# Kernel optimization log

Hardware: AMD Instinct MI355X
Metric: run time of the kernel (lower is better)

Reference implementation:

```python
import jax, jax.numpy as jnp
import numpy as np

D_MODEL = 512
NUM_HEADS = 8
HEAD_DIM = D_MODEL // NUM_HEADS
NUM_Z_BINS = 16
MAX_Z = 5.0
N = 2048


def setup_inputs() -> dict:
    key = jax.random.key(0)
    ks = jax.random.split(key, 12)
    s = 1.0 / np.sqrt(D_MODEL)
    return {
        "x": jax.random.normal(ks[0], (N, D_MODEL), dtype=jnp.float32),
        "z_matrix": jax.random.uniform(ks[1], (N, N), dtype=jnp.float32),
        "Wq": jax.random.normal(ks[2], (D_MODEL, D_MODEL), dtype=jnp.float32) * s,
        "bq": jnp.zeros((D_MODEL,), dtype=jnp.float32),
        "Wk": jax.random.normal(ks[3], (D_MODEL, D_MODEL), dtype=jnp.float32) * s,
        "bk": jnp.zeros((D_MODEL,), dtype=jnp.float32),
        "Wv": jax.random.normal(ks[4], (D_MODEL, D_MODEL), dtype=jnp.float32) * s,
        "bv": jnp.zeros((D_MODEL,), dtype=jnp.float32),
        "Wo": jax.random.normal(ks[5], (D_MODEL, D_MODEL), dtype=jnp.float32) * s,
        "bo": jnp.zeros((D_MODEL,), dtype=jnp.float32),
        "z_table": jax.random.normal(ks[6], (NUM_Z_BINS, NUM_HEADS), dtype=jnp.float32) * 0.02,
    }


def reference(x, z_matrix, Wq, bq, Wk, bk, Wv, bv, Wo, bo, z_table):
    n = x.shape[0]
    scale = HEAD_DIM ** -0.5
    q = (x @ Wq + bq).reshape(n, NUM_HEADS, HEAD_DIM)
    k = (x @ Wk + bk).reshape(n, NUM_HEADS, HEAD_DIM)
    v = (x @ Wv + bv).reshape(n, NUM_HEADS, HEAD_DIM)
    # [n, h, m] attention scores
    scores = jnp.einsum('nhd,mhd->nhm', q, k) * scale
    # Z-bus relative bias: bin pairwise z values into NUM_Z_BINS over [0, MAX_Z],
    # look up per-head bias from the embedding table.
    bins = jnp.clip(jnp.floor(z_matrix / MAX_Z * NUM_Z_BINS).astype(jnp.int32), 0, NUM_Z_BINS - 1)
    bias = z_table[bins]                    # [n, n, h]
    scores = scores + jnp.transpose(bias, (0, 2, 1))  # [n, h, n]
    attn = jax.nn.softmax(scores, axis=-1)  # dropout p=0.0 (eval)
    out = jnp.einsum('nhm,mhd->nhd', attn, v).reshape(n, D_MODEL)
    return out @ Wo + bo
```

## Files before the change

### kernel.cpp

```cpp
#include <hip/hip_runtime.h>
#include <hip/hip_bf16.h>


#define NTOK   2048
#define DM     512
#define NH     8
#define DH     64
#define NBINS  16
#define NSPLIT 4
#define KPS    (NTOK / NSPLIT)

typedef float  f32x16 __attribute__((ext_vector_type(16)));
typedef short  short8 __attribute__((ext_vector_type(8)));
typedef unsigned short ushort_t;

#define MFMA32(A, B, C) __builtin_amdgcn_mfma_f32_32x32x16_bf16((A), (B), (C), 0, 0, 0)

__device__ __forceinline__ ushort_t f2bf(float x) {
    __hip_bfloat16 h = __float2bfloat16(x);
    union { __hip_bfloat16 b; ushort_t u; } v; v.b = h;
    return v.u;
}
__device__ __forceinline__ float bf2f(ushort_t b) {
    union { unsigned u; float f; } v; v.u = ((unsigned)b) << 16;
    return v.f;
}
__device__ __forceinline__ void splitbf(float x, ushort_t& hi, ushort_t& lo) {
    hi = f2bf(x);
    lo = f2bf(x - bf2f(hi));
}

union FragU { unsigned u[4]; short8 s; };

__device__ __forceinline__ int z_to_bin(float z) {
    int b = (int)floorf(z / 5.0f * 16.0f);
    return b < 0 ? 0 : (b > 15 ? 15 : b);
}

__global__ __launch_bounds__(256)
void prep_all(const float* __restrict__ z, unsigned char* __restrict__ bins,
              const float* __restrict__ x, ushort_t* __restrict__ xh, ushort_t* __restrict__ xl,
              const float* __restrict__ Wq, const float* __restrict__ Wk,
              const float* __restrict__ Wv, const float* __restrict__ Wo,
              ushort_t* __restrict__ wt_hi_base, ushort_t* __restrict__ wt_lo_base) {
    const int bid = blockIdx.x;
    const int t   = threadIdx.x;
    __shared__ float Tl[32][33];

    if (bid < 4096) {
        int i = (bid * 256 + t) * 4;
        float4 zv = *reinterpret_cast<const float4*>(z + i);
        uchar4 b;
        b.x = (unsigned char)z_to_bin(zv.x);
        b.y = (unsigned char)z_to_bin(zv.y);
        b.z = (unsigned char)z_to_bin(zv.z);
        b.w = (unsigned char)z_to_bin(zv.w);
        *reinterpret_cast<uchar4*>(bins + i) = b;
    } else if (bid < 5120) {
        int i = ((bid - 4096) * 256 + t) * 4;
        float4 v = *reinterpret_cast<const float4*>(x + i);
        ushort_t h[4], l[4];
        splitbf(v.x, h[0], l[0]); splitbf(v.y, h[1], l[1]);
        splitbf(v.z, h[2], l[2]); splitbf(v.w, h[3], l[3]);
        *reinterpret_cast<ushort4*>(xh + i) = make_ushort4(h[0], h[1], h[2], h[3]);
        *reinterpret_cast<ushort4*>(xl + i) = make_ushort4(l[0], l[1], l[2], l[3]);
    } else {
        const int pz  = bid - 5120;
        const int zz  = pz >> 8;
        const int rem = pz & 255;
        const float* __restrict__ W = zz == 0 ? Wq : zz == 1 ? Wk : zz == 2 ? Wv : Wo;
        ushort_t* __restrict__ th = wt_hi_base + (size_t)zz * DM * DM * 2;
        ushort_t* __restrict__ tl = wt_lo_base + (size_t)zz * DM * DM * 2;
        const int r0 = (rem >> 4) * 32;
        const int c0 = (rem & 15) * 32;
        {
            const int r = t >> 3, c4 = (t & 7) * 4;
            float4 v = *reinterpret_cast<const float4*>(W + (size_t)(r0 + r) * DM + c0 + c4);
            Tl[r][c4 + 0] = v.x; Tl[r][c4 + 1] = v.y; Tl[r][c4 + 2] = v.z; Tl[r][c4 + 3] = v.w;
        }
        __syncthreads();
        {
            const int c = t >> 3, r4 = (t & 7) * 4;
            ushort_t h4[4], l4[4];
            #pragma unroll
            for (int k = 0; k < 4; ++k) splitbf(Tl[r4 + k][c], h4[k], l4[k]);
            *reinterpret_cast<ushort4*>(th + (size_t)(c0 + c) * DM + r0 + r4) =
                make_ushort4(h4[0], h4[1], h4[2], h4[3]);
            *reinterpret_cast<ushort4*>(tl + (size_t)(c0 + c) * DM + r0 + r4) =
                make_ushort4(l4[0], l4[1], l4[2], l4[3]);
        }
    }
}

__global__ __launch_bounds__(256, 3)
void qkv_gemm_mfma(const ushort_t* __restrict__ x_hi, const ushort_t* __restrict__ x_lo,
                   const ushort_t* __restrict__ wqt_hi, const ushort_t* __restrict__ wqt_lo,
                   const ushort_t* __restrict__ wkt_hi, const ushort_t* __restrict__ wkt_lo,
                   const ushort_t* __restrict__ wvt_hi, const ushort_t* __restrict__ wvt_lo,
                   const float* __restrict__ bq, const float* __restrict__ bk,
                   const float* __restrict__ bv,
                   ushort_t* __restrict__ q_hi, ushort_t* __restrict__ q_lo,
                   ushort_t* __restrict__ k_hi, ushort_t* __restrict__ k_lo,
                   ushort_t* __restrict__ vT_hi, ushort_t* __restrict__ vT_lo) {
    const int z = blockIdx.z;
    const ushort_t* __restrict__ bt_hi = z == 0 ? wqt_hi : z == 1 ? wkt_hi : wvt_hi;
    const ushort_t* __restrict__ bt_lo = z == 0 ? wqt_lo : z == 1 ? wkt_lo : wvt_lo;
    const float*    __restrict__ bias  = z == 0 ? bq : z == 1 ? bk : bv;

    const int n0 = blockIdx.x * 64;
    const int m0 = blockIdx.y * 64;
    const int t  = threadIdx.x;
    const int wid = t >> 6, l = t & 63, hf = l >> 5, lq = l & 31;
    const int wm = wid >> 1, wn = wid & 1;

    __shared__ __align__(16) ushort_t Ash_hi[64 * 40], Ash_lo[64 * 40];
    __shared__ __align__(16) ushort_t Bsh_hi[64 * 40], Bsh_lo[64 * 40];

    f32x16 acc;
    #pragma unroll
    for (int i = 0; i < 16; ++i) acc[i] = 0.0f;

    const int sr = t >> 2, sc = t & 3;

    uint4 ra_h, ra_l, rb_h, rb_l;
    auto LOAD = [&](int k0) {
        ra_h = *reinterpret_cast<const uint4*>(&x_hi[(size_t)(m0 + sr) * DM + k0 + 8 * sc]);
        ra_l = *reinterpret_cast<const uint4*>(&x_lo[(size_t)(m0 + sr) * DM + k0 + 8 * sc]);
        rb_h = *reinterpret_cast<const uint4*>(&bt_hi[(size_t)(n0 + sr) * DM + k0 + 8 * sc]);
        rb_l = *reinterpret_cast<const uint4*>(&bt_lo[(size_t)(n0 + sr) * DM + k0 + 8 * sc]);
    };
    LOAD(0);

    for (int k0 = 0; k0 < DM; k0 += 32) {
        __syncthreads();
        *reinterpret_cast<uint4*>(&Ash_hi[sr * 40 + 8 * sc]) = ra_h;
        *reinterpret_cast<uint4*>(&Ash_lo[sr * 40 + 8 * sc]) = ra_l;
        *reinterpret_cast<uint4*>(&Bsh_hi[sr * 40 + 8 * sc]) = rb_h;
        *reinterpret_cast<uint4*>(&Bsh_lo[sr * 40 + 8 * sc]) = rb_l;
        __syncthreads();
        if (k0 + 32 < DM) LOAD(k0 + 32);

        __builtin_amdgcn_s_setprio(1);
        #pragma unroll
        for (int kp = 0; kp < 2; ++kp) {
            const int co = 8 * (hf + 2 * kp);
            short8 ah = *reinterpret_cast<const short8*>(&Ash_hi[(32 * wm + lq) * 40 + co]);
            short8 al = *reinterpret_cast<const short8*>(&Ash_lo[(32 * wm + lq) * 40 + co]);
            short8 bh = *reinterpret_cast<const short8*>(&Bsh_hi[(32 * wn + lq) * 40 + co]);
            short8 bl = *reinterpret_cast<const short8*>(&Bsh_lo[(32 * wn + lq) * 40 + co]);
            acc = MFMA32(ah, bh, acc);
            acc = MFMA32(ah, bl, acc);
            acc = MFMA32(al, bh, acc);
        }
        __builtin_amdgcn_s_setprio(0);
    }

    const int nl = lq + 32 * wn;
    const float bval = bias[n0 + nl];
    const int hh = n0 >> 6;

    #pragma unroll
    for (int r = 0; r < 16; ++r) {
        const int ml = (r & 3) + 8 * (r >> 2) + 4 * hf + 32 * wm;
        const float v = acc[r] + bval;
        ushort_t hi, lo; splitbf(v, hi, lo);
        if (z < 2) {
            ushort_t* dh = z == 0 ? q_hi : k_hi;
            ushort_t* dl = z == 0 ? q_lo : k_lo;
            const size_t o = ((size_t)hh * NTOK + m0 + ml) * DH + nl;
            dh[o] = hi; dl[o] = lo;
        } else {
            const size_t o = ((size_t)hh * DH + nl) * NTOK + m0 + ml;
            vT_hi[o] = hi; vT_lo[o] = lo;
        }
    }
}

__global__ __launch_bounds__(256, 3)
void wo_gemm_mfma(const ushort_t* __restrict__ a_hi, const ushort_t* __restrict__ a_lo,
                  const ushort_t* __restrict__ bt_hi, const ushort_t* __restrict__ bt_lo,
                  const float* __restrict__ bias, float* __restrict__ out) {
    const int n0 = blockIdx.x * 64;
    const int m0 = blockIdx.y * 64;
    const int t  = threadIdx.x;
    const int wid = t >> 6, l = t & 63, hf = l >> 5, lq = l & 31;
    const int wm = wid >> 1, wn = wid & 1;

    __shared__ __align__(16) ushort_t Ash_hi[64 * 40], Ash_lo[64 * 40];
    __shared__ __align__(16) ushort_t Bsh_hi[64 * 40], Bsh_lo[64 * 40];

    f32x16 acc;
    #pragma unroll
    for (int i = 0; i < 16; ++i) acc[i] = 0.0f;

    const int sr = t >> 2, sc = t & 3;

    uint4 ra_h, ra_l, rb_h, rb_l;
    auto LOAD = [&](int k0) {
        ra_h = *reinterpret_cast<const uint4*>(&a_hi[(size_t)(m0 + sr) * DM + k0 + 8 * sc]);
        ra_l = *reinterpret_cast<const uint4*>(&a_lo[(size_t)(m0 + sr) * DM + k0 + 8 * sc]);
        rb_h = *reinterpret_cast<const uint4*>(&bt_hi[(size_t)(n0 + sr) * DM + k0 + 8 * sc]);
        rb_l = *reinterpret_cast<const uint4*>(&bt_lo[(size_t)(n0 + sr) * DM + k0 + 8 * sc]);
    };
    LOAD(0);

    for (int k0 = 0; k0 < DM; k0 += 32) {
        __syncthreads();
        *reinterpret_cast<uint4*>(&Ash_hi[sr * 40 + 8 * sc]) = ra_h;
        *reinterpret_cast<uint4*>(&Ash_lo[sr * 40 + 8 * sc]) = ra_l;
        *reinterpret_cast<uint4*>(&Bsh_hi[sr * 40 + 8 * sc]) = rb_h;
        *reinterpret_cast<uint4*>(&Bsh_lo[sr * 40 + 8 * sc]) = rb_l;
        __syncthreads();
        if (k0 + 32 < DM) LOAD(k0 + 32);

        __builtin_amdgcn_s_setprio(1);
        #pragma unroll
        for (int kp = 0; kp < 2; ++kp) {
            const int co = 8 * (hf + 2 * kp);
            short8 ah = *reinterpret_cast<const short8*>(&Ash_hi[(32 * wm + lq) * 40 + co]);
            short8 al = *reinterpret_cast<const short8*>(&Ash_lo[(32 * wm + lq) * 40 + co]);
            short8 bh = *reinterpret_cast<const short8*>(&Bsh_hi[(32 * wn + lq) * 40 + co]);
            short8 bl = *reinterpret_cast<const short8*>(&Bsh_lo[(32 * wn + lq) * 40 + co]);
            acc = MFMA32(ah, bh, acc);
            acc = MFMA32(ah, bl, acc);
            acc = MFMA32(al, bh, acc);
        }
        __builtin_amdgcn_s_setprio(0);
    }

    const int nl = lq + 32 * wn;
    const float bval = bias[n0 + nl];
    #pragma unroll
    for (int r = 0; r < 16; ++r) {
        const int ml = (r & 3) + 8 * (r >> 2) + 4 * hf + 32 * wm;
        out[(size_t)(m0 + ml) * DM + n0 + nl] = acc[r] + bval;
    }
}

__global__ __launch_bounds__(256, 2)
void attn_mfma(const ushort_t* __restrict__ q_hi, const ushort_t* __restrict__ q_lo,
               const ushort_t* __restrict__ k_hi, const ushort_t* __restrict__ k_lo,
               const ushort_t* __restrict__ vT_hi, const ushort_t* __restrict__ vT_lo,
               const unsigned char* __restrict__ bins_g, const float* __restrict__ z_table,
               float* __restrict__ po, float* __restrict__ pm, float* __restrict__ pl) {
    const int hd = blockIdx.y;
    const int q0 = blockIdx.x * 128;
    const int zs = blockIdx.z;
    const int t  = threadIdx.x;
    const int wid = t >> 6, l = t & 63, hf = l >> 5, lq = l & 31;
    const int qs = q0 + 32 * wid;

    __shared__ __align__(16) ushort_t Ksh_hi[64 * 72], Ksh_lo[64 * 72];
    __shared__ __align__(16) ushort_t Vsh_hi[64 * 72], Vsh_lo[64 * 72];
    __shared__ __align__(16) unsigned char Bsh[128 * 80];

    const float ztab = z_table[(l & 15) * NH + hd];

    short8 qf_hi[4], qf_lo[4];
    #pragma unroll
    for (int kp = 0; kp < 4; ++kp) {
        const size_t o = ((size_t)hd * NTOK + qs + lq) * DH + 8 * hf + 16 * kp;
        qf_hi[kp] = *reinterpret_cast<const short8*>(&q_hi[o]);
        qf_lo[kp] = *reinterpret_cast<const short8*>(&q_lo[o]);
    }

    float m_run = -1e30f, l_run = 0.0f;
    f32x16 oacc0, oacc1;
    #pragma unroll
    for (int i = 0; i < 16; ++i) { oacc0[i] = 0.0f; oacc1[i] = 0.0f; }

    const float scale = 0.125f;
    const int kbase = zs * KPS;

    for (int kt8 = 0; kt8 < KPS / 64; ++kt8) {
        const int ktb = kbase + kt8 * 64;
        __syncthreads();
        #pragma unroll
        for (int i = 0; i < 2; ++i) {
            const int idx = t + 256 * i;
            const int r = idx >> 3, c = idx & 7;
            const size_t kg = ((size_t)hd * NTOK + ktb + r) * DH + 8 * c;
            const size_t vg = ((size_t)hd * DH + r) * NTOK + ktb + 8 * c;
            *reinterpret_cast<uint4*>(&Ksh_hi[r * 72 + 8 * c]) =
                *reinterpret_cast<const uint4*>(&k_hi[kg]);
            *reinterpret_cast<uint4*>(&Ksh_lo[r * 72 + 8 * c]) =
                *reinterpret_cast<const uint4*>(&k_lo[kg]);
            *reinterpret_cast<uint4*>(&Vsh_hi[r * 72 + 8 * c]) =
                *reinterpret_cast<const uint4*>(&vT_hi[vg]);
            *reinterpret_cast<uint4*>(&Vsh_lo[r * 72 + 8 * c]) =
                *reinterpret_cast<const uint4*>(&vT_lo[vg]);
        }
        #pragma unroll
        for (int i = 0; i < 2; ++i) {
            const int idx = t + 256 * i;
            const int qr = idx >> 2, c = idx & 3;
            *reinterpret_cast<uint4*>(&Bsh[qr * 80 + 16 * c]) =
                *reinterpret_cast<const uint4*>(&bins_g[(size_t)(q0 + qr) * NTOK + ktb + 16 * c]);
        }
        __syncthreads();

        f32x16 sacc0, sacc1;
        #pragma unroll
        for (int i = 0; i < 16; ++i) { sacc0[i] = 0.0f; sacc1[i] = 0.0f; }
        __builtin_amdgcn_s_setprio(1);
        #pragma unroll
        for (int kp = 0; kp < 4; ++kp) {
            const int co = 8 * (hf + 2 * kp);
            short8 k0h = *reinterpret_cast<const short8*>(&Ksh_hi[lq * 72 + co]);
            short8 k0l = *reinterpret_cast<const short8*>(&Ksh_lo[lq * 72 + co]);
            short8 k1h = *reinterpret_cast<const short8*>(&Ksh_hi[(lq + 32) * 72 + co]);
            short8 k1l = *reinterpret_cast<const short8*>(&Ksh_lo[(lq + 32) * 72 + co]);
            sacc0 = MFMA32(k0h, qf_hi[kp], sacc0);
            sacc0 = MFMA32(k0h, qf_lo[kp], sacc0);
            sacc0 = MFMA32(k0l, qf_hi[kp], sacc0);
            sacc1 = MFMA32(k1h, qf_hi[kp], sacc1);
            sacc1 = MFMA32(k1h, qf_lo[kp], sacc1);
            sacc1 = MFMA32(k1l, qf_hi[kp], sacc1);
        }
        __builtin_amdgcn_s_setprio(0);

        float sv[2][16];
        #pragma unroll
        for (int t2 = 0; t2 < 2; ++t2) {
            #pragma unroll
            for (int b = 0; b < 4; ++b) {
                const unsigned bw = *reinterpret_cast<const unsigned*>(
                    &Bsh[(32 * wid + lq) * 80 + 4 * (hf + 2 * b + 8 * t2)]);
                #pragma unroll
                for (int c = 0; c < 4; ++c) {
                    const int r = c + 4 * b;
                    const int src = (int)((bw >> (8 * c)) & 0xFF) | (l & 48);
                    const float bias = __shfl(ztab, src, 64);
                    const float sraw = (t2 == 0 ? sacc0[r] : sacc1[r]);
                    sv[t2][r] = sraw * scale + bias;
                }
            }
        }

        float tm = sv[0][0];
        #pragma unroll
        for (int t2 = 0; t2 < 2; ++t2)
            #pragma unroll
            for (int r = 0; r < 16; ++r) tm = fmaxf(tm, sv[t2][r]);
        tm = fmaxf(tm, __shfl_xor(tm, 32, 64));
        const float mn = fmaxf(m_run, tm);
        const float ef = __expf(m_run - mn);
        m_run = mn;

        float pv[2][16];
        float ts = 0.0f;
        #pragma unroll
        for (int t2 = 0; t2 < 2; ++t2)
            #pragma unroll
            for (int r = 0; r < 16; ++r) {
                const float p = __expf(sv[t2][r] - mn);
                pv[t2][r] = p;
                ts += p;
            }
        ts += __shfl_xor(ts, 32, 64);
        l_run = l_run * ef + ts;

        #pragma unroll
        for (int r = 0; r < 16; ++r) {
            const int qloc = (r & 3) + 8 * (r >> 2) + 4 * hf;
            const float efr = __shfl(ef, qloc | (l & 32), 64);
            oacc0[r] *= efr;
            oacc1[r] *= efr;
        }

        unsigned phi[2][8], plo[2][8];
        #pragma unroll
        for (int t2 = 0; t2 < 2; ++t2)
            #pragma unroll
            for (int i = 0; i < 8; ++i) {
                ushort_t ha, la, hb, lb;
                splitbf(pv[t2][2 * i],     ha, la);
                splitbf(pv[t2][2 * i + 1], hb, lb);
                phi[t2][i] = (unsigned)ha | ((unsigned)hb << 16);
                plo[t2][i] = (unsigned)la | ((unsigned)lb << 16);
            }

        FragU paf_hi[2][2], paf_lo[2][2];
        #pragma unroll
        for (int t2 = 0; t2 < 2; ++t2)
            #pragma unroll
            for (int e = 0; e < 2; ++e) {
                {
                    const unsigned pA0 = phi[t2][4 * e], pA1 = phi[t2][4 * e + 1];
                    const unsigned pB0 = phi[t2][4 * e + 2], pB1 = phi[t2][4 * e + 3];
                    const unsigned s0 = hf ? pA0 : pB0, s1 = hf ? pA1 : pB1;
                    const unsigned r0 = (unsigned)__shfl_xor((int)s0, 32, 64);
                    const unsigned r1 = (unsigned)__shfl_xor((int)s1, 32, 64);
                    paf_hi[t2][e].u[0] = hf ? r0 : pA0;
                    paf_hi[t2][e].u[1] = hf ? r1 : pA1;
                    paf_hi[t2][e].u[2] = hf ? pB0 : r0;
                    paf_hi[t2][e].u[3] = hf ? pB1 : r1;
                }
                {
                    const unsigned pA0 = plo[t2][4 * e], pA1 = plo[t2][4 * e + 1];
                    const unsigned pB0 = plo[t2][4 * e + 2], pB1 = plo[t2][4 * e + 3];
                    const unsigned s0 = hf ? pA0 : pB0, s1 = hf ? pA1 : pB1;
                    const unsigned r0 = (unsigned)__shfl_xor((int)s0, 32, 64);
                    const unsigned r1 = (unsigned)__shfl_xor((int)s1, 32, 64);
                    paf_lo[t2][e].u[0] = hf ? r0 : pA0;
                    paf_lo[t2][e].u[1] = hf ? r1 : pA1;
                    paf_lo[t2][e].u[2] = hf ? pB0 : r0;
                    paf_lo[t2][e].u[3] = hf ? pB1 : r1;
                }
            }

        __builtin_amdgcn_s_setprio(1);
        #pragma unroll
        for (int kp = 0; kp < 4; ++kp) {
            const int t2 = kp >> 1, e = kp & 1;
            const int co = 8 * (hf + 2 * kp);
            short8 v0h = *reinterpret_cast<const short8*>(&Vsh_hi[lq * 72 + co]);
            short8 v0l = *reinterpret_cast<const short8*>(&Vsh_lo[lq * 72 + co]);
            oacc0 = MFMA32(paf_hi[t2][e].s, v0h, oacc0);
            oacc0 = MFMA32(paf_hi[t2][e].s, v0l, oacc0);
            oacc0 = MFMA32(paf_lo[t2][e].s, v0h, oacc0);
            short8 v1h = *reinterpret_cast<const short8*>(&Vsh_hi[(lq + 32) * 72 + co]);
            short8 v1l = *reinterpret_cast<const short8*>(&Vsh_lo[(lq + 32) * 72 + co]);
            oacc1 = MFMA32(paf_hi[t2][e].s, v1h, oacc1);
            oacc1 = MFMA32(paf_hi[t2][e].s, v1l, oacc1);
            oacc1 = MFMA32(paf_lo[t2][e].s, v1h, oacc1);
        }
        __builtin_amdgcn_s_setprio(0);
    }

    #pragma unroll
    for (int r = 0; r < 16; ++r) {
        const int qloc = (r & 3) + 8 * (r >> 2) + 4 * hf;
        const size_t row = ((size_t)(zs * NH + hd) * NTOK + qs + qloc) * DH;
        po[row + lq]      = oacc0[r];
        po[row + lq + 32] = oacc1[r];
    }
    if (hf == 0) {
        const size_t row = (size_t)(zs * NH + hd) * NTOK + qs + lq;
        pm[row] = m_run;
        pl[row] = l_run;
    }
}

__global__ __launch_bounds__(256)
void merge_kernel(const float* __restrict__ po, const float* __restrict__ pm,
                  const float* __restrict__ pl,
                  ushort_t* __restrict__ o_hi, ushort_t* __restrict__ o_lo) {
    const int idx = blockIdx.x * 256 + threadIdx.x;
    const int d4 = (idx & 15) * 4;
    const int q  = (idx >> 4) & (NTOK - 1);
    const int hh = idx >> 15;

    float ms[NSPLIT];
    float M = -1e30f;
    #pragma unroll
    for (int s = 0; s < NSPLIT; ++s) {
        ms[s] = pm[((size_t)s * NH + hh) * NTOK + q];
        M = fmaxf(M, ms[s]);
    }
    float L = 0.0f;
    float4 o = make_float4(0.f, 0.f, 0.f, 0.f);
    #pragma unroll
    for (int s = 0; s < NSPLIT; ++s) {
        const float w = __expf(ms[s] - M);
        L += w * pl[((size_t)s * NH + hh) * NTOK + q];
        float4 p = *reinterpret_cast<const float4*>(
            po + (((size_t)s * NH + hh) * NTOK + q) * DH + d4);
        o.x += w * p.x; o.y += w * p.y; o.z += w * p.z; o.w += w * p.w;
    }
    const float inv = 1.0f / L;
    o.x *= inv; o.y *= inv; o.z *= inv; o.w *= inv;

    ushort_t h4[4], l4[4];
    splitbf(o.x, h4[0], l4[0]); splitbf(o.y, h4[1], l4[1]);
    splitbf(o.z, h4[2], l4[2]); splitbf(o.w, h4[3], l4[3]);
    const size_t oo = (size_t)q * DM + hh * DH + d4;
    *reinterpret_cast<ushort4*>(o_hi + oo) = make_ushort4(h4[0], h4[1], h4[2], h4[3]);
    *reinterpret_cast<ushort4*>(o_lo + oo) = make_ushort4(l4[0], l4[1], l4[2], l4[3]);
}

extern "C" void kernel_launch(void* const* d_in, const int* in_sizes, int n_in,
                              void* d_out, int out_size, void* d_ws, size_t ws_size,
                              hipStream_t stream) {
    const float* x        = (const float*)d_in[0];
    const float* z_matrix = (const float*)d_in[1];
    const float* Wq       = (const float*)d_in[2];
    const float* bq       = (const float*)d_in[3];
    const float* Wk       = (const float*)d_in[4];
    const float* bk       = (const float*)d_in[5];
    const float* Wv       = (const float*)d_in[6];
    const float* bv       = (const float*)d_in[7];
    const float* Wo       = (const float*)d_in[8];
    const float* bo       = (const float*)d_in[9];
    const float* z_table  = (const float*)d_in[10];
    float* out            = (float*)d_out;

    uint8_t* w = (uint8_t*)d_ws;
    const size_t MB = 1024 * 1024;
    ushort_t* x_hi  = (ushort_t*)(w + 0);
    ushort_t* x_lo  = (ushort_t*)(w + 2  * MB);
    ushort_t* wqt_hi= (ushort_t*)(w + 4  * MB);
    ushort_t* wqt_lo= (ushort_t*)(w + 4  * MB + 512 * 1024);
    ushort_t* wkt_hi= (ushort_t*)(w + 5  * MB);
    ushort_t* wkt_lo= (ushort_t*)(w + 5  * MB + 512 * 1024);
    ushort_t* wvt_hi= (ushort_t*)(w + 6  * MB);
    ushort_t* wvt_lo= (ushort_t*)(w + 6  * MB + 512 * 1024);
    ushort_t* wot_hi= (ushort_t*)(w + 7  * MB);
    ushort_t* wot_lo= (ushort_t*)(w + 7  * MB + 512 * 1024);
    ushort_t* q_hi  = (ushort_t*)(w + 8  * MB);
    ushort_t* q_lo  = (ushort_t*)(w + 10 * MB);
    ushort_t* k_hi  = (ushort_t*)(w + 12 * MB);
    ushort_t* k_lo  = (ushort_t*)(w + 14 * MB);
    ushort_t* vT_hi = (ushort_t*)(w + 16 * MB);
    ushort_t* vT_lo = (ushort_t*)(w + 18 * MB);
    unsigned char* bins = (unsigned char*)(w + 20 * MB);
    float* po = (float*)(w + 24 * MB);
    float* pm = (float*)(w + 40 * MB);
    float* pl = (float*)(w + 40 * MB + 256 * 1024);
    ushort_t* o_hi = x_hi;
    ushort_t* o_lo = x_lo;

    prep_all<<<dim3(4096 + 1024 + 1024), dim3(256), 0, stream>>>(
        z_matrix, bins, x, x_hi, x_lo, Wq, Wk, Wv, Wo,
        (ushort_t*)(w + 4 * MB), (ushort_t*)(w + 4 * MB + 512 * 1024));

    qkv_gemm_mfma<<<dim3(DM / 64, NTOK / 64, 3), dim3(256), 0, stream>>>(
        x_hi, x_lo,
        wqt_hi, wqt_lo, wkt_hi, wkt_lo, wvt_hi, wvt_lo,
        bq, bk, bv,
        q_hi, q_lo, k_hi, k_lo, vT_hi, vT_lo);

    attn_mfma<<<dim3(NTOK / 128, NH, NSPLIT), dim3(256), 0, stream>>>(
        q_hi, q_lo, k_hi, k_lo, vT_hi, vT_lo, bins, z_table, po, pm, pl);

    merge_kernel<<<dim3(NH * NTOK * DH / 4 / 256), dim3(256), 0, stream>>>(
        po, pm, pl, o_hi, o_lo);

    wo_gemm_mfma<<<dim3(DM / 64, NTOK / 64), dim3(256), 0, stream>>>(
        o_hi, o_lo, wot_hi, wot_lo, bo, out);
}
```

Before: 164.6 us.

## Lazy softmax rescale, raise occupancy, and use 8-way KV split when workspace allows

Adds a lazy online-softmax update: when no row's tile max exceeds the running max by more than 8, the rescale of the output accumulators and of l is skipped, which removes shuffles and multiplies from the common path. The split count becomes a template parameter and rises from 4 to 8 when the workspace holds at least 58 MB, giving more blocks per head. Launch bounds go from 2 to 3 blocks per SM. The costs are more partial-output traffic in the merge, possible register spills under the tighter launch bound, and a larger workspace requirement.

```diff
diff --git a/kernel.cpp b/kernel.cpp
--- a/kernel.cpp
+++ b/kernel.cpp
@@ -7,8 +7,6 @@
 #define NH     8
 #define DH     64
 #define NBINS  16
-#define NSPLIT 4
-#define KPS    (NTOK / NSPLIT)
 
 typedef float  f32x16 __attribute__((ext_vector_type(16)));
 typedef short  short8 __attribute__((ext_vector_type(8)));
@@ -237,12 +235,14 @@
     }
 }
 
-__global__ __launch_bounds__(256, 2)
+template<int NS>
+__global__ __launch_bounds__(256, 3)
 void attn_mfma(const ushort_t* __restrict__ q_hi, const ushort_t* __restrict__ q_lo,
                const ushort_t* __restrict__ k_hi, const ushort_t* __restrict__ k_lo,
                const ushort_t* __restrict__ vT_hi, const ushort_t* __restrict__ vT_lo,
                const unsigned char* __restrict__ bins_g, const float* __restrict__ z_table,
                float* __restrict__ po, float* __restrict__ pm, float* __restrict__ pl) {
+    constexpr int KPS = NTOK / NS;
     const int hd = blockIdx.y;
     const int q0 = blockIdx.x * 128;
     const int zs = blockIdx.z;
@@ -343,9 +343,14 @@
             #pragma unroll
             for (int r = 0; r < 16; ++r) tm = fmaxf(tm, sv[t2][r]);
         tm = fmaxf(tm, __shfl_xor(tm, 32, 64));
-        const float mn = fmaxf(m_run, tm);
-        const float ef = __expf(m_run - mn);
-        m_run = mn;
+
+        const bool defer = __all(tm <= m_run + 8.0f);
+        float ef = 0.0f;
+        if (!defer) {
+            const float mn = fmaxf(m_run, tm);
+            ef = __expf(m_run - mn);
+            m_run = mn;
+        }
 
         float pv[2][16];
         float ts = 0.0f;
@@ -353,19 +358,23 @@
         for (int t2 = 0; t2 < 2; ++t2)
             #pragma unroll
             for (int r = 0; r < 16; ++r) {
-                const float p = __expf(sv[t2][r] - mn);
+                const float p = __expf(sv[t2][r] - m_run);
                 pv[t2][r] = p;
                 ts += p;
             }
         ts += __shfl_xor(ts, 32, 64);
-        l_run = l_run * ef + ts;
-
-        #pragma unroll
-        for (int r = 0; r < 16; ++r) {
-            const int qloc = (r & 3) + 8 * (r >> 2) + 4 * hf;
-            const float efr = __shfl(ef, qloc | (l & 32), 64);
-            oacc0[r] *= efr;
-            oacc1[r] *= efr;
+
+        if (defer) {
+            l_run += ts;
+        } else {
+            l_run = l_run * ef + ts;
+            #pragma unroll
+            for (int r = 0; r < 16; ++r) {
+                const int qloc = (r & 3) + 8 * (r >> 2) + 4 * hf;
+                const float efr = __shfl(ef, qloc | (l & 32), 64);
+                oacc0[r] *= efr;
+                oacc1[r] *= efr;
+            }
         }
 
         unsigned phi[2][8], plo[2][8];
@@ -442,6 +451,7 @@
     }
 }
 
+template<int NS>
 __global__ __launch_bounds__(256)
 void merge_kernel(const float* __restrict__ po, const float* __restrict__ pm,
                   const float* __restrict__ pl,
@@ -451,17 +461,17 @@
     const int q  = (idx >> 4) & (NTOK - 1);
     const int hh = idx >> 15;
 
-    float ms[NSPLIT];
+    float ms[NS];
     float M = -1e30f;
     #pragma unroll
-    for (int s = 0; s < NSPLIT; ++s) {
+    for (int s = 0; s < NS; ++s) {
         ms[s] = pm[((size_t)s * NH + hh) * NTOK + q];
         M = fmaxf(M, ms[s]);
     }
     float L = 0.0f;
     float4 o = make_float4(0.f, 0.f, 0.f, 0.f);
     #pragma unroll
-    for (int s = 0; s < NSPLIT; ++s) {
+    for (int s = 0; s < NS; ++s) {
         const float w = __expf(ms[s] - M);
         L += w * pl[((size_t)s * NH + hh) * NTOK + q];
         float4 p = *reinterpret_cast<const float4*>(
@@ -514,11 +524,13 @@
     ushort_t* vT_hi = (ushort_t*)(w + 16 * MB);
     ushort_t* vT_lo = (ushort_t*)(w + 18 * MB);
     unsigned char* bins = (unsigned char*)(w + 20 * MB);
-    float* po = (float*)(w + 24 * MB);
-    float* pm = (float*)(w + 40 * MB);
-    float* pl = (float*)(w + 40 * MB + 256 * 1024);
     ushort_t* o_hi = x_hi;
     ushort_t* o_lo = x_lo;
+
+    const int ns = (ws_size >= 58 * MB) ? 8 : 4;
+    float* po = (float*)(w + 24 * MB);
+    float* pm = po + (size_t)ns * NH * NTOK * DH;
+    float* pl = pm + (size_t)ns * NH * NTOK;
 
     prep_all<<<dim3(4096 + 1024 + 1024), dim3(256), 0, stream>>>(
         z_matrix, bins, x, x_hi, x_lo, Wq, Wk, Wv, Wo,
@@ -530,11 +542,17 @@
         bq, bk, bv,
         q_hi, q_lo, k_hi, k_lo, vT_hi, vT_lo);
 
-    attn_mfma<<<dim3(NTOK / 128, NH, NSPLIT), dim3(256), 0, stream>>>(
-        q_hi, q_lo, k_hi, k_lo, vT_hi, vT_lo, bins, z_table, po, pm, pl);
-
-    merge_kernel<<<dim3(NH * NTOK * DH / 4 / 256), dim3(256), 0, stream>>>(
-        po, pm, pl, o_hi, o_lo);
+    if (ns == 8) {
+        attn_mfma<8><<<dim3(NTOK / 128, NH, 8), dim3(256), 0, stream>>>(
+            q_hi, q_lo, k_hi, k_lo, vT_hi, vT_lo, bins, z_table, po, pm, pl);
+        merge_kernel<8><<<dim3(NH * NTOK * DH / 4 / 256), dim3(256), 0, stream>>>(
+            po, pm, pl, o_hi, o_lo);
+    } else {
+        attn_mfma<4><<<dim3(NTOK / 128, NH, 4), dim3(256), 0, stream>>>(
+            q_hi, q_lo, k_hi, k_lo, vT_hi, vT_lo, bins, z_table, po, pm, pl);
+        merge_kernel<4><<<dim3(NH * NTOK * DH / 4 / 256), dim3(256), 0, stream>>>(
+            po, pm, pl, o_hi, o_lo);
+    }
 
     wo_gemm_mfma<<<dim3(DM / 64, NTOK / 64), dim3(256), 0, stream>>>(
         o_hi, o_lo, wot_hi, wot_lo, bo, out);
```

Result: slower. 184.7 us (+12.3%).
